# Kernel optimization log

Hardware: AMD Instinct MI355X
Metric: run time of the kernel (lower is better)

## Reference

```python
import jax, jax.numpy as jnp
import numpy as np

N_NODES = 50000
N_EDGES = 600000
D_IN = 128
D_OUT = 128
LN_EPS = 1e-5


def setup_inputs() -> dict:
    key = jax.random.key(0)
    ks = jax.random.split(key, 12)
    x = jax.random.normal(ks[0], (N_NODES, D_IN), dtype=jnp.float32)
    adj_in_rows = jax.random.randint(ks[1], (N_EDGES,), 0, N_NODES, dtype=jnp.int32)
    adj_in_cols = jax.random.randint(ks[2], (N_EDGES,), 0, N_NODES, dtype=jnp.int32)
    adj_in_vals = jax.random.uniform(ks[3], (N_EDGES,), dtype=jnp.float32)
    adj_out_rows = jax.random.randint(ks[4], (N_EDGES,), 0, N_NODES, dtype=jnp.int32)
    adj_out_cols = jax.random.randint(ks[5], (N_EDGES,), 0, N_NODES, dtype=jnp.int32)
    adj_out_vals = jax.random.uniform(ks[6], (N_EDGES,), dtype=jnp.float32)
    s = 1.0 / np.sqrt(D_IN)
    W_self = jax.random.uniform(ks[7], (D_OUT, D_IN), dtype=jnp.float32, minval=-s, maxval=s)
    b_self = jax.random.uniform(ks[8], (D_OUT,), dtype=jnp.float32, minval=-s, maxval=s)
    W_in = jax.random.uniform(ks[9], (D_OUT, D_IN), dtype=jnp.float32, minval=-s, maxval=s)
    W_out = jax.random.uniform(ks[10], (D_OUT, D_IN), dtype=jnp.float32, minval=-s, maxval=s)
    ln_gamma = jnp.ones((D_OUT,), dtype=jnp.float32)
    ln_beta = jnp.zeros((D_OUT,), dtype=jnp.float32)
    return {
        "x": x,
        "adj_in_rows": adj_in_rows, "adj_in_cols": adj_in_cols, "adj_in_vals": adj_in_vals,
        "adj_out_rows": adj_out_rows, "adj_out_cols": adj_out_cols, "adj_out_vals": adj_out_vals,
        "W_self": W_self, "b_self": b_self, "W_in": W_in, "W_out": W_out,
        "ln_gamma": ln_gamma, "ln_beta": ln_beta,
    }


def _spmm(rows, cols, vals, x, n):
    # COO sparse.mm: out[r] += vals[e] * x[cols[e]]
    return jax.ops.segment_sum(vals[:, None] * x[cols], rows, num_segments=n)


def reference(x, adj_in_rows, adj_in_cols, adj_in_vals,
              adj_out_rows, adj_out_cols, adj_out_vals,
              W_self, b_self, W_in, W_out, ln_gamma, ln_beta):
    n = x.shape[0]
    agg_in = _spmm(adj_in_rows, adj_in_cols, adj_in_vals, x, n)
    agg_out = _spmm(adj_out_rows, adj_out_cols, adj_out_vals, x, n)
    h = x @ W_self.T + b_self + agg_in @ W_in.T + agg_out @ W_out.T
    mu = jnp.mean(h, axis=-1, keepdims=True)
    var = jnp.mean(jnp.square(h - mu), axis=-1, keepdims=True)
    h = (h - mu) * jax.lax.rsqrt(var + LN_EPS) * ln_gamma + ln_beta
    # dropout is identity in eval mode (training=False)
    return jax.nn.relu(h)
```

## Files before the change

kernel.cpp:

```cpp
#include <hip/hip_runtime.h>

#define N_NODES 50000
#define N_EDGES 600000
#define D 128
#define BM 32
#define NT (2 * N_NODES)
#define NE2 (2 * N_EDGES)
#define NPAD 50048
#define KA 384
#define GBM 64
#define NB 1563
#define BROWS 64
#define CAPE 1024
#define CHUNK_A 8192

typedef __attribute__((ext_vector_type(8))) short bf16x8;
typedef __attribute__((ext_vector_type(4))) float f32x4;

__device__ inline unsigned short bfr(float x) {
    unsigned b = __float_as_uint(x);
    b += 0x7FFFu + ((b >> 16) & 1u);
    return (unsigned short)(b >> 16);
}
__device__ inline float bf_lo(unsigned u) { return __uint_as_float(u << 16); }
__device__ inline float bf_hi(unsigned u) { return __uint_as_float(u & 0xFFFF0000u); }


__global__ __launch_bounds__(256) void cvt_x(const float* __restrict__ x, short* __restrict__ A)
{
    int gid = blockIdx.x * 256 + threadIdx.x;
    if (gid >= N_NODES * 32) return;
    int row = gid >> 5, c4 = gid & 31;
    float4 v = *reinterpret_cast<const float4*>(x + (size_t)row * D + c4 * 4);
    ushort4 o = { bfr(v.x), bfr(v.y), bfr(v.z), bfr(v.w) };
    *reinterpret_cast<ushort4*>(A + (size_t)row * KA + c4 * 4) = o;
}

__global__ __launch_bounds__(384) void cvt_w(
    const float* __restrict__ Ws, const float* __restrict__ Wi,
    const float* __restrict__ Wo, short* __restrict__ Wc)
{
    int j = blockIdx.x, k = threadIdx.x;
    float v = (k < 128) ? Ws[j * 128 + k]
            : (k < 256) ? Wi[j * 128 + k - 128]
                        : Wo[j * 128 + k - 256];
    Wc[j * KA + k] = (short)bfr(v);
}


__global__ __launch_bounds__(1024) void bucket_hist(
    const int* __restrict__ ir, const int* __restrict__ orow, int* __restrict__ bcnt)
{
    __shared__ int h[NB];
    for (int i = threadIdx.x; i < NB; i += 1024) h[i] = 0;
    __syncthreads();
    int stride = gridDim.x * 1024;
    for (int e = blockIdx.x * 1024 + threadIdx.x; e < NE2; e += stride) {
        int r = (e < N_EDGES) ? ir[e] : N_NODES + orow[e - N_EDGES];
        atomicAdd(&h[r >> 6], 1);
    }
    __syncthreads();
    for (int i = threadIdx.x; i < NB; i += 1024)
        if (h[i]) atomicAdd(&bcnt[i], h[i]);
}

__global__ __launch_bounds__(1024) void scan_buckets(
    const int* __restrict__ bcnt, int* __restrict__ bbase, int* __restrict__ bcur)
{
    __shared__ int s[1024];
    const int t = threadIdx.x;
    const int i0 = 2 * t, i1 = 2 * t + 1;
    int v0 = (i0 < NB) ? bcnt[i0] : 0;
    int v1 = (i1 < NB) ? bcnt[i1] : 0;
    int v = v0 + v1;
    s[t] = v;
    __syncthreads();
    for (int o = 1; o < 1024; o <<= 1) {
        int u = (t >= o) ? s[t - o] : 0;
        __syncthreads();
        s[t] += u;
        __syncthreads();
    }
    int ex = s[t] - v;
    if (i0 < NB) { bbase[i0] = ex;      bcur[i0] = ex; }
    if (i1 < NB) { bbase[i1] = ex + v0; bcur[i1] = ex + v0; }
}

__global__ __launch_bounds__(1024) void scatter_buckets(
    const int* __restrict__ ir, const int* __restrict__ icol, const float* __restrict__ ival,
    const int* __restrict__ orow, const int* __restrict__ ocol, const float* __restrict__ oval,
    int* __restrict__ bcur, int2* __restrict__ pairp)
{
    __shared__ int hist[NB];
    __shared__ int cur[NB];
    const int t = threadIdx.x;
    for (int i = t; i < NB; i += 1024) hist[i] = 0;
    __syncthreads();

    const int e0 = blockIdx.x * CHUNK_A;
    int rr[8], cc[8]; float vv[8];
#pragma unroll
    for (int i = 0; i < 8; ++i) {
        int e = e0 + t + i * 1024;
        if (e < N_EDGES)      { rr[i] = ir[e];                       cc[i] = icol[e];           vv[i] = ival[e]; }
        else if (e < NE2)     { rr[i] = N_NODES + orow[e - N_EDGES]; cc[i] = ocol[e - N_EDGES]; vv[i] = oval[e - N_EDGES]; }
        else                  { rr[i] = -1; cc[i] = 0; vv[i] = 0.f; }
        if (rr[i] >= 0) atomicAdd(&hist[rr[i] >> 6], 1);
    }
    __syncthreads();
    for (int i = t; i < NB; i += 1024) {
        int c = hist[i];
        cur[i] = c ? atomicAdd(&bcur[i], c) : 0;
    }
    __syncthreads();
#pragma unroll
    for (int i = 0; i < 8; ++i) {
        if (rr[i] < 0) continue;
        int pos = atomicAdd(&cur[rr[i] >> 6], 1);
        pairp[pos] = make_int2((cc[i] & 0xFFFF) | ((rr[i] & 63) << 16), __float_as_int(vv[i]));
    }
}

__global__ __launch_bounds__(256) void bucket_spmm(
    const int* __restrict__ bbase, const int* __restrict__ bcnt,
    const int2* __restrict__ pairp, short* __restrict__ A)
{
    __shared__ int2 ed[CAPE];
    __shared__ int  rs[BROWS];
    __shared__ int  rstart[BROWS + 1];
    __shared__ int  rcur[BROWS];

    const int t = threadIdx.x;
    const int b = blockIdx.x;
    const int base = bbase[b];
    const int n = bcnt[b];
    const int w = t >> 6, lane = t & 63;
    const int row0 = w * 16;
    const char* Ab = (const char*)A + lane * 4;

    float ax[16], ay[16];
#pragma unroll
    for (int i = 0; i < 16; ++i) { ax[i] = 0.f; ay[i] = 0.f; }

    for (int s0 = 0; s0 < n; s0 += CAPE) {
        const int m = min(n - s0, CAPE);
        if (t < BROWS) rs[t] = 0;
        __syncthreads();
        int2 myp[4];
#pragma unroll
        for (int k = 0; k < 4; ++k) {
            int i = t + k * 256;
            if (i < m) {
                myp[k] = pairp[base + s0 + i];
                atomicAdd(&rs[(myp[k].x >> 16) & 63], 1);
            }
        }
        __syncthreads();
        if (t < 64) {
            int v = rs[t];
            int acc = v;
#pragma unroll
            for (int o = 1; o < 64; o <<= 1) {
                int u = __shfl_up(acc, o);
                if (t >= o) acc += u;
            }
            rstart[t] = acc - v;
            rcur[t]   = acc - v;
            if (t == 63) rstart[64] = acc;
        }
        __syncthreads();
#pragma unroll
        for (int k = 0; k < 4; ++k) {
            int i = t + k * 256;
            if (i < m) {
                int pos = atomicAdd(&rcur[(myp[k].x >> 16) & 63], 1);
                ed[pos] = myp[k];
            }
        }
        __syncthreads();
#pragma unroll
        for (int ri = 0; ri < 16; ++ri) {
            const int r = row0 + ri;
            int i = rstart[r];
            const int e2 = rstart[r + 1];
            float lax = ax[ri], lay = ay[ri];
            for (; i + 3 < e2; i += 4) {
                int2 p0 = ed[i], p1 = ed[i + 1], p2 = ed[i + 2], p3 = ed[i + 3];
                unsigned u0 = *(const unsigned*)(Ab + (unsigned)((p0.x & 0xFFFF) * (KA * 2)));
                unsigned u1 = *(const unsigned*)(Ab + (unsigned)((p1.x & 0xFFFF) * (KA * 2)));
                unsigned u2 = *(const unsigned*)(Ab + (unsigned)((p2.x & 0xFFFF) * (KA * 2)));
                unsigned u3 = *(const unsigned*)(Ab + (unsigned)((p3.x & 0xFFFF) * (KA * 2)));
                float v0 = __int_as_float(p0.y), v1 = __int_as_float(p1.y);
                float v2 = __int_as_float(p2.y), v3 = __int_as_float(p3.y);
                lax += v0 * bf_lo(u0) + v1 * bf_lo(u1) + v2 * bf_lo(u2) + v3 * bf_lo(u3);
                lay += v0 * bf_hi(u0) + v1 * bf_hi(u1) + v2 * bf_hi(u2) + v3 * bf_hi(u3);
            }
            for (; i < e2; ++i) {
                int2 p = ed[i];
                float v = __int_as_float(p.y);
                unsigned u = *(const unsigned*)(Ab + (unsigned)((p.x & 0xFFFF) * (KA * 2)));
                lax += v * bf_lo(u);
                lay += v * bf_hi(u);
            }
            ax[ri] = lax; ay[ri] = lay;
        }
        __syncthreads();
    }

    char* Aw = (char*)A;
#pragma unroll
    for (int ri = 0; ri < 16; ++ri) {
        int wv = b * BROWS + row0 + ri;
        if (wv >= NT) continue;
        unsigned o = ((unsigned)bfr(ay[ri]) << 16) | (unsigned)bfr(ax[ri]);
        size_t dst = (wv < N_NODES)
                   ? ((size_t)wv * (KA * 2) + 256 + lane * 4)
                   : ((size_t)(wv - N_NODES) * (KA * 2) + 512 + lane * 4);
        *(unsigned*)(Aw + dst) = o;
    }
}

__global__ __launch_bounds__(512) void gemm_mfma(
    const short* __restrict__ A, const short* __restrict__ Wc,
    const float* __restrict__ b, const float* __restrict__ gamma,
    const float* __restrict__ beta, float* __restrict__ out)
{
    __shared__ short Alds[GBM * KA];
    __shared__ float red[8][64][2];
    __shared__ float2 mustd[64];

    const int t = threadIdx.x;
    const int l = t & 63, w = t >> 6;
    const int q = l >> 4, c = l & 15;
    const int base = blockIdx.x * GBM;

    bf16x8 bfrag[12];
    const short* wrow = Wc + (size_t)(w * 16 + c) * KA + q * 8;
#pragma unroll
    for (int s = 0; s < 12; ++s)
        bfrag[s] = *reinterpret_cast<const bf16x8*>(wrow + s * 32);

#pragma unroll
    for (int i = 0; i < 6; ++i) {
        int slot = t + i * 512;
        int row = slot / 48, c16 = slot % 48;
        bf16x8 v = *reinterpret_cast<const bf16x8*>(A + (size_t)(base + row) * KA + c16 * 8);
        *reinterpret_cast<bf16x8*>(&Alds[row * KA + (c16 ^ (row & 7)) * 8]) = v;
    }
    __syncthreads();

    f32x4 acc[4];
#pragma unroll
    for (int rg = 0; rg < 4; ++rg) acc[rg] = (f32x4){0.f, 0.f, 0.f, 0.f};

#pragma unroll
    for (int s = 0; s < 12; ++s) {
#pragma unroll
        for (int rg = 0; rg < 4; ++rg) {
            int row = rg * 16 + c;
            int c16 = (s * 4 + q) ^ (row & 7);
            bf16x8 af = *reinterpret_cast<const bf16x8*>(&Alds[row * KA + c16 * 8]);
            acc[rg] = __builtin_amdgcn_mfma_f32_16x16x32_bf16(af, bfrag[s], acc[rg], 0, 0, 0);
        }
    }

    const float bj = b[w * 16 + c];
    const float gj = gamma[w * 16 + c];
    const float ej = beta[w * 16 + c];

#pragma unroll
    for (int rg = 0; rg < 4; ++rg) {
#pragma unroll
        for (int r = 0; r < 4; ++r) {
            float hv = acc[rg][r] + bj;
            acc[rg][r] = hv;
            float s1 = hv, s2 = hv * hv;
#pragma unroll
            for (int m = 1; m < 16; m <<= 1) {
                s1 += __shfl_xor(s1, m);
                s2 += __shfl_xor(s2, m);
            }
            if (c == 0) {
                int row = rg * 16 + q * 4 + r;
                red[w][row][0] = s1;
                red[w][row][1] = s2;
            }
        }
    }
    __syncthreads();

    if (t < 64) {
        float s1 = 0.f, s2 = 0.f;
#pragma unroll
        for (int ww = 0; ww < 8; ++ww) { s1 += red[ww][t][0]; s2 += red[ww][t][1]; }
        float mu = s1 * (1.f / 128.f);
        float var = s2 * (1.f / 128.f) - mu * mu;
        mustd[t] = make_float2(mu, rsqrtf(var + 1e-5f));
    }
    __syncthreads();

#pragma unroll
    for (int rg = 0; rg < 4; ++rg) {
        int row0 = rg * 16 + q * 4;
        int node0 = base + row0;
#pragma unroll
        for (int r = 0; r < 4; ++r) {
            float2 ms = mustd[row0 + r];
            float y = (acc[rg][r] - ms.x) * ms.y * gj + ej;
            y = fmaxf(y, 0.f);
            if (node0 + r < N_NODES)
                out[(size_t)(node0 + r) * D + w * 16 + c] = y;
        }
    }
}

__global__ __launch_bounds__(256) void spmm_scatter(
    const int* __restrict__ rows, const int* __restrict__ cols,
    const float* __restrict__ vals, const float* __restrict__ x,
    float* __restrict__ agg, int nE)
{
    int g = blockIdx.x * 256 + threadIdx.x;
    int e = g >> 5;
    if (e >= nE) return;
    int q = g & 31;
    int r = rows[e], c = cols[e];
    float v = vals[e];
    float4 xv = *reinterpret_cast<const float4*>(x + (size_t)c * D + (size_t)q * 4);
    float* ap = agg + (size_t)r * D + (size_t)q * 4;
    atomicAdd(ap + 0, v * xv.x);
    atomicAdd(ap + 1, v * xv.y);
    atomicAdd(ap + 2, v * xv.z);
    atomicAdd(ap + 3, v * xv.w);
}

__global__ __launch_bounds__(256) void gemm_ln_relu(
    const float* __restrict__ x, const float* __restrict__ agg_in,
    const float* __restrict__ agg_out,
    const float* __restrict__ Ws, const float* __restrict__ Wi,
    const float* __restrict__ Wo, const float* __restrict__ b,
    const float* __restrict__ gamma, const float* __restrict__ beta,
    float* __restrict__ out, int n)
{
    __shared__ float4 Wl[D * (D / 4)];
    __shared__ float4 Xl[BM * (D / 4)];

    const int t = threadIdx.x;
    const int l = t & 63;
    const int w = t >> 6;
    const int base = blockIdx.x * BM;
    const int j0 = l, j1 = l + 64;

    float acc0[8], acc1[8];
    const float bj0 = b[j0], bj1 = b[j1];
#pragma unroll
    for (int i = 0; i < 8; ++i) { acc0[i] = bj0; acc1[i] = bj1; }

    const float* srcs[3] = { x, agg_in, agg_out };
    const float* wms[3]  = { Ws, Wi, Wo };

#pragma unroll
    for (int s = 0; s < 3; ++s) {
        const float4* src4 = reinterpret_cast<const float4*>(srcs[s]);
        const float4* w4   = reinterpret_cast<const float4*>(wms[s]);
        __syncthreads();
#pragma unroll
        for (int it = 0; it < 16; ++it) {
            int gi = t + 256 * it;
            int j = gi >> 5, k4 = gi & 31;
            Wl[j * 32 + (k4 ^ (j & 7))] = w4[gi];
        }
#pragma unroll
        for (int it = 0; it < 4; ++it) {
            int gi = t + 256 * it;
            int m = gi >> 5, k4 = gi & 31;
            int node = base + m;
            float4 v = (node < n) ? src4[(size_t)node * 32 + k4]
                                  : make_float4(0.f, 0.f, 0.f, 0.f);
            Xl[m * 32 + k4] = v;
        }
        __syncthreads();

        const int sw = j0 & 7;
#pragma unroll 8
        for (int k4 = 0; k4 < 32; ++k4) {
            float4 w0 = Wl[j0 * 32 + (k4 ^ sw)];
            float4 w1 = Wl[j1 * 32 + (k4 ^ sw)];
#pragma unroll
            for (int i = 0; i < 8; ++i) {
                float4 xv = Xl[(w + 4 * i) * 32 + k4];
                acc0[i] += xv.x * w0.x + xv.y * w0.y + xv.z * w0.z + xv.w * w0.w;
                acc1[i] += xv.x * w1.x + xv.y * w1.y + xv.z * w1.z + xv.w * w1.w;
            }
        }
    }

    const float g0 = gamma[j0], g1 = gamma[j1];
    const float be0 = beta[j0], be1 = beta[j1];
#pragma unroll
    for (int i = 0; i < 8; ++i) {
        int node = base + w + 4 * i;
        float s  = acc0[i] + acc1[i];
        float ss = acc0[i] * acc0[i] + acc1[i] * acc1[i];
#pragma unroll
        for (int off = 32; off; off >>= 1) {
            s  += __shfl_xor(s, off);
            ss += __shfl_xor(ss, off);
        }
        float mu   = s * (1.0f / D);
        float var  = ss * (1.0f / D) - mu * mu;
        float rstd = rsqrtf(var + 1e-5f);
        if (node < n) {
            float y0 = (acc0[i] - mu) * rstd * g0 + be0;
            float y1 = (acc1[i] - mu) * rstd * g1 + be1;
            out[(size_t)node * D + j0] = fmaxf(y0, 0.f);
            out[(size_t)node * D + j1] = fmaxf(y1, 0.f);
        }
    }
}

extern "C" void kernel_launch(void* const* d_in, const int* in_sizes, int n_in,
                              void* d_out, int out_size, void* d_ws, size_t ws_size,
                              hipStream_t stream) {
    const float* x     = (const float*)d_in[0];
    const int*   ir    = (const int*)  d_in[1];
    const int*   icoln = (const int*)  d_in[2];
    const float* ival  = (const float*)d_in[3];
    const int*   orow  = (const int*)  d_in[4];
    const int*   ocol  = (const int*)  d_in[5];
    const float* oval  = (const float*)d_in[6];
    const float* Ws    = (const float*)d_in[7];
    const float* b     = (const float*)d_in[8];
    const float* Wi    = (const float*)d_in[9];
    const float* Wo    = (const float*)d_in[10];
    const float* gamma = (const float*)d_in[11];
    const float* beta  = (const float*)d_in[12];
    float* out = (float*)d_out;

    short* A     = (short*)d_ws;
    short* Wc    = A + (size_t)NPAD * KA;
    int*   bcnt  = (int*)(Wc + (size_t)128 * KA);
    int*   bbase = bcnt + NB;
    int*   bcur  = bbase + NB;
    int2*  pairp = (int2*)(bcur + NB + ((3 * NB) & 1));
    size_t need  = (size_t)NPAD * KA * 2 + (size_t)128 * KA * 2
                 + (size_t)(3 * NB + 2) * 4 + (size_t)NE2 * 8;

    if (ws_size >= need) {
        hipMemsetAsync(bcnt, 0, NB * sizeof(int), stream);
        hipMemsetAsync(A + (size_t)N_NODES * KA, 0,
                       (size_t)(NPAD - N_NODES) * KA * 2, stream);

        cvt_x<<<(N_NODES * 32 + 255) / 256, 256, 0, stream>>>(x, A);
        cvt_w<<<128, 384, 0, stream>>>(Ws, Wi, Wo, Wc);

        bucket_hist<<<128, 1024, 0, stream>>>(ir, orow, bcnt);
        scan_buckets<<<1, 1024, 0, stream>>>(bcnt, bbase, bcur);
        scatter_buckets<<<(NE2 + CHUNK_A - 1) / CHUNK_A, 1024, 0, stream>>>(
            ir, icoln, ival, orow, ocol, oval, bcur, pairp);
        bucket_spmm<<<NB, 256, 0, stream>>>(bbase, bcnt, pairp, A);

        gemm_mfma<<<NPAD / GBM, 512, 0, stream>>>(A, Wc, b, gamma, beta, out);
    } else {
        float* agg_in  = (float*)d_ws;
        float* agg_out = agg_in + (size_t)N_NODES * D;
        hipMemsetAsync(d_ws, 0, 2 * (size_t)N_NODES * D * sizeof(float), stream);
        const int eblocks = (N_EDGES * 32 + 255) / 256;
        spmm_scatter<<<eblocks, 256, 0, stream>>>(ir, icoln, ival, x, agg_in, N_EDGES);
        spmm_scatter<<<eblocks, 256, 0, stream>>>(orow, ocol, oval, x, agg_out, N_EDGES);
        const int gblocks = (N_NODES + BM - 1) / BM;
        gemm_ln_relu<<<gblocks, 256, 0, stream>>>(x, agg_in, agg_out, Ws, Wi, Wo,
                                                  b, gamma, beta, out, N_NODES);
    }
}
```

Before: 145.5 us.

## Stage bucket scatter in LDS and widen SpMM gathers to 8-byte loads

scatter_buckets now sorts each chunk's edges by bucket in shared memory, using a block-local scan and a per-bucket global base, then writes the pairs out in bucket order, so global stores land in contiguous runs instead of random positions. bucket_spmm moves to 512 threads: each wave covers 8 rows, and its two half-waves split a row's edges, each lane loading 4 bf16 features (8 bytes) per edge, with the halves combined by a cross-half shuffle. The aim is better coalescing on both scatter writes and gathers, at the cost of more shared memory (about 100KB in scatter) and some wasted, clamped loads on rows with few edges.

```diff
diff --git a/kernel.cpp b/kernel.cpp
--- a/kernel.cpp
+++ b/kernel.cpp
@@ -91,13 +91,19 @@
     const int* __restrict__ orow, const int* __restrict__ ocol, const float* __restrict__ oval,
     int* __restrict__ bcur, int2* __restrict__ pairp)
 {
-    __shared__ int hist[NB];
-    __shared__ int cur[NB];
+    __shared__ int2 pay[CHUNK_A];
+    __shared__ int  dstp[CHUNK_A];
+    __shared__ int  hist[NB];
+    __shared__ int  lofs[NB];
+    __shared__ int  gb2[NB];
+    __shared__ int  sbuf[1024];
+
     const int t = threadIdx.x;
     for (int i = t; i < NB; i += 1024) hist[i] = 0;
     __syncthreads();
 
     const int e0 = blockIdx.x * CHUNK_A;
+    const int m = min(NE2 - e0, CHUNK_A);
     int rr[8], cc[8]; float vv[8];
 #pragma unroll
     for (int i = 0; i < 8; ++i) {
@@ -108,20 +114,48 @@
         if (rr[i] >= 0) atomicAdd(&hist[rr[i] >> 6], 1);
     }
     __syncthreads();
+
+    const int i0 = 2 * t, i1 = 2 * t + 1;
+    int h0 = (i0 < NB) ? hist[i0] : 0;
+    int h1 = (i1 < NB) ? hist[i1] : 0;
+    int hv = h0 + h1;
+    sbuf[t] = hv;
+    __syncthreads();
+    for (int o = 1; o < 1024; o <<= 1) {
+        int u = (t >= o) ? sbuf[t - o] : 0;
+        __syncthreads();
+        sbuf[t] += u;
+        __syncthreads();
+    }
+    int ex = sbuf[t] - hv;
+    if (i0 < NB) lofs[i0] = ex;
+    if (i1 < NB) lofs[i1] = ex + h0;
+    __syncthreads();
+
     for (int i = t; i < NB; i += 1024) {
         int c = hist[i];
-        cur[i] = c ? atomicAdd(&bcur[i], c) : 0;
-    }
-    __syncthreads();
+        int g = c ? atomicAdd(&bcur[i], c) : 0;
+        gb2[i] = g - lofs[i];
+    }
+    __syncthreads();
+    for (int i = t; i < NB; i += 1024) hist[i] = lofs[i];
+    __syncthreads();
+
 #pragma unroll
     for (int i = 0; i < 8; ++i) {
         if (rr[i] < 0) continue;
-        int pos = atomicAdd(&cur[rr[i] >> 6], 1);
-        pairp[pos] = make_int2((cc[i] & 0xFFFF) | ((rr[i] & 63) << 16), __float_as_int(vv[i]));
-    }
-}
-
-__global__ __launch_bounds__(256) void bucket_spmm(
+        int bk = rr[i] >> 6;
+        int s = atomicAdd(&hist[bk], 1);
+        pay[s]  = make_int2((cc[i] & 0xFFFF) | ((rr[i] & 63) << 16), __float_as_int(vv[i]));
+        dstp[s] = gb2[bk] + s;
+    }
+    __syncthreads();
+
+    for (int i = t; i < m; i += 1024)
+        pairp[dstp[i]] = pay[i];
+}
+
+__global__ __launch_bounds__(512) void bucket_spmm(
     const int* __restrict__ bbase, const int* __restrict__ bcnt,
     const int2* __restrict__ pairp, short* __restrict__ A)
 {
@@ -135,21 +169,22 @@
     const int base = bbase[b];
     const int n = bcnt[b];
     const int w = t >> 6, lane = t & 63;
-    const int row0 = w * 16;
-    const char* Ab = (const char*)A + lane * 4;
-
-    float ax[16], ay[16];
-#pragma unroll
-    for (int i = 0; i < 16; ++i) { ax[i] = 0.f; ay[i] = 0.f; }
+    const int h = lane >> 5, sl = lane & 31;
+    const int row0 = w * 8;
+    const char* Ab = (const char*)A + sl * 8;
+
+    float4 acc[8];
+#pragma unroll
+    for (int i = 0; i < 8; ++i) acc[i] = make_float4(0.f, 0.f, 0.f, 0.f);
 
     for (int s0 = 0; s0 < n; s0 += CAPE) {
         const int m = min(n - s0, CAPE);
         if (t < BROWS) rs[t] = 0;
         __syncthreads();
-        int2 myp[4];
-#pragma unroll
-        for (int k = 0; k < 4; ++k) {
-            int i = t + k * 256;
+        int2 myp[2];
+#pragma unroll
+        for (int k = 0; k < 2; ++k) {
+            int i = t + k * 512;
             if (i < m) {
                 myp[k] = pairp[base + s0 + i];
                 atomicAdd(&rs[(myp[k].x >> 16) & 63], 1);
@@ -158,20 +193,20 @@
         __syncthreads();
         if (t < 64) {
             int v = rs[t];
-            int acc = v;
+            int a = v;
 #pragma unroll
             for (int o = 1; o < 64; o <<= 1) {
-                int u = __shfl_up(acc, o);
-                if (t >= o) acc += u;
-            }
-            rstart[t] = acc - v;
-            rcur[t]   = acc - v;
-            if (t == 63) rstart[64] = acc;
-        }
-        __syncthreads();
-#pragma unroll
-        for (int k = 0; k < 4; ++k) {
-            int i = t + k * 256;
+                int u = __shfl_up(a, o);
+                if (t >= o) a += u;
+            }
+            rstart[t] = a - v;
+            rcur[t]   = a - v;
+            if (t == 63) rstart[64] = a;
+        }
+        __syncthreads();
+#pragma unroll
+        for (int k = 0; k < 2; ++k) {
+            int i = t + k * 512;
             if (i < m) {
                 int pos = atomicAdd(&rcur[(myp[k].x >> 16) & 63], 1);
                 ed[pos] = myp[k];
@@ -179,44 +214,46 @@
         }
         __syncthreads();
 #pragma unroll
-        for (int ri = 0; ri < 16; ++ri) {
+        for (int ri = 0; ri < 8; ++ri) {
             const int r = row0 + ri;
-            int i = rstart[r];
-            const int e2 = rstart[r + 1];
-            float lax = ax[ri], lay = ay[ri];
-            for (; i + 3 < e2; i += 4) {
-                int2 p0 = ed[i], p1 = ed[i + 1], p2 = ed[i + 2], p3 = ed[i + 3];
-                unsigned u0 = *(const unsigned*)(Ab + (unsigned)((p0.x & 0xFFFF) * (KA * 2)));
-                unsigned u1 = *(const unsigned*)(Ab + (unsigned)((p1.x & 0xFFFF) * (KA * 2)));
-                unsigned u2 = *(const unsigned*)(Ab + (unsigned)((p2.x & 0xFFFF) * (KA * 2)));
-                unsigned u3 = *(const unsigned*)(Ab + (unsigned)((p3.x & 0xFFFF) * (KA * 2)));
-                float v0 = __int_as_float(p0.y), v1 = __int_as_float(p1.y);
-                float v2 = __int_as_float(p2.y), v3 = __int_as_float(p3.y);
-                lax += v0 * bf_lo(u0) + v1 * bf_lo(u1) + v2 * bf_lo(u2) + v3 * bf_lo(u3);
-                lay += v0 * bf_hi(u0) + v1 * bf_hi(u1) + v2 * bf_hi(u2) + v3 * bf_hi(u3);
-            }
-            for (; i < e2; ++i) {
-                int2 p = ed[i];
-                float v = __int_as_float(p.y);
-                unsigned u = *(const unsigned*)(Ab + (unsigned)((p.x & 0xFFFF) * (KA * 2)));
-                lax += v * bf_lo(u);
-                lay += v * bf_hi(u);
-            }
-            ax[ri] = lax; ay[ri] = lay;
+            const int s = rstart[r], e2 = rstart[r + 1];
+            float4 a = acc[ri];
+            for (int i = s; i < e2; i += 8) {
+#pragma unroll
+                for (int k = 0; k < 4; ++k) {
+                    int idx = i + 2 * k + h;
+                    int2 p = ed[min(idx, e2 - 1)];
+                    float v = (idx < e2) ? __int_as_float(p.y) : 0.f;
+                    uint2 u = *(const uint2*)(Ab + (unsigned)((p.x & 0xFFFF) * (KA * 2)));
+                    a.x += v * bf_lo(u.x);
+                    a.y += v * bf_hi(u.x);
+                    a.z += v * bf_lo(u.y);
+                    a.w += v * bf_hi(u.y);
+                }
+            }
+            acc[ri] = a;
         }
         __syncthreads();
     }
 
     char* Aw = (char*)A;
 #pragma unroll
-    for (int ri = 0; ri < 16; ++ri) {
+    for (int ri = 0; ri < 8; ++ri) {
+        float4 a = acc[ri];
+        a.x += __shfl_xor(a.x, 32);
+        a.y += __shfl_xor(a.y, 32);
+        a.z += __shfl_xor(a.z, 32);
+        a.w += __shfl_xor(a.w, 32);
         int wv = b * BROWS + row0 + ri;
-        if (wv >= NT) continue;
-        unsigned o = ((unsigned)bfr(ay[ri]) << 16) | (unsigned)bfr(ax[ri]);
-        size_t dst = (wv < N_NODES)
-                   ? ((size_t)wv * (KA * 2) + 256 + lane * 4)
-                   : ((size_t)(wv - N_NODES) * (KA * 2) + 512 + lane * 4);
-        *(unsigned*)(Aw + dst) = o;
+        if (lane < 32 && wv < NT) {
+            uint2 o;
+            o.x = ((unsigned)bfr(a.y) << 16) | (unsigned)bfr(a.x);
+            o.y = ((unsigned)bfr(a.w) << 16) | (unsigned)bfr(a.z);
+            size_t dst = (wv < N_NODES)
+                       ? ((size_t)wv * (KA * 2) + 256 + sl * 8)
+                       : ((size_t)(wv - N_NODES) * (KA * 2) + 512 + sl * 8);
+            *(uint2*)(Aw + dst) = o;
+        }
     }
 }
 
@@ -457,7 +494,7 @@
         scan_buckets<<<1, 1024, 0, stream>>>(bcnt, bbase, bcur);
         scatter_buckets<<<(NE2 + CHUNK_A - 1) / CHUNK_A, 1024, 0, stream>>>(
             ir, icoln, ival, orow, ocol, oval, bcur, pairp);
-        bucket_spmm<<<NB, 256, 0, stream>>>(bbase, bcnt, pairp, A);
+        bucket_spmm<<<NB, 512, 0, stream>>>(bbase, bcnt, pairp, A);
 
         gemm_mfma<<<NPAD / GBM, 512, 0, stream>>>(A, Wc, b, gamma, beta, out);
     } else {
```

Measured after the change: 137.9 us. -5.3%, faster.

## Split bucket SpMM into row sort plus wave-per-row gather, coalesce scatter

Applied to the files above, without the earlier changes.

The fused bucket SpMM kernel, where each wave walked 16 rows serially, is replaced by two kernels. A row_sort kernel builds a per-row CSR (row_ptr plus sorted pairs), and a gather_rows kernel gives each row its own wave, with an 8-way unrolled gather loop. The edge scatter now does a local counting sort of each chunk in LDS, so global writes go out grouped by bucket instead of as random single stores. The x and weight conversions and the zeroing memsets are folded into one prep kernel to cut launch count. The cost is an extra kernel launch and an extra full pass over the edge pair array, plus more workspace.

```diff
diff --git a/kernel.cpp b/kernel.cpp
--- a/kernel.cpp
+++ b/kernel.cpp
@@ -9,10 +9,9 @@
 #define NPAD 50048
 #define KA 384
 #define GBM 64
-#define NB 1563
-#define BROWS 64
-#define CAPE 1024
-#define CHUNK_A 8192
+#define NBB 1563
+#define CAPB 2048
+#define CHUNK_A 4096
 
 typedef __attribute__((ext_vector_type(8))) short bf16x8;
 typedef __attribute__((ext_vector_type(4))) float f32x4;
@@ -25,42 +24,59 @@
 __device__ inline float bf_lo(unsigned u) { return __uint_as_float(u << 16); }
 __device__ inline float bf_hi(unsigned u) { return __uint_as_float(u & 0xFFFF0000u); }
 
-
-__global__ __launch_bounds__(256) void cvt_x(const float* __restrict__ x, short* __restrict__ A)
-{
-    int gid = blockIdx.x * 256 + threadIdx.x;
-    if (gid >= N_NODES * 32) return;
-    int row = gid >> 5, c4 = gid & 31;
-    float4 v = *reinterpret_cast<const float4*>(x + (size_t)row * D + c4 * 4);
-    ushort4 o = { bfr(v.x), bfr(v.y), bfr(v.z), bfr(v.w) };
-    *reinterpret_cast<ushort4*>(A + (size_t)row * KA + c4 * 4) = o;
-}
-
-__global__ __launch_bounds__(384) void cvt_w(
-    const float* __restrict__ Ws, const float* __restrict__ Wi,
-    const float* __restrict__ Wo, short* __restrict__ Wc)
-{
-    int j = blockIdx.x, k = threadIdx.x;
-    float v = (k < 128) ? Ws[j * 128 + k]
-            : (k < 256) ? Wi[j * 128 + k - 128]
-                        : Wo[j * 128 + k - 256];
-    Wc[j * KA + k] = (short)bfr(v);
+#define G1 (NPAD * 32 / 256)
+#define G2 192
+#define NZI (NBB + 48 * 128)
+#define G3 ((NZI + 255) / 256)
+
+__global__ __launch_bounds__(256) void prep(
+    const float* __restrict__ x, const float* __restrict__ Ws,
+    const float* __restrict__ Wi, const float* __restrict__ Wo,
+    short* __restrict__ A, short* __restrict__ Wc, int* __restrict__ bcnt)
+{
+    const int bid = blockIdx.x, t = threadIdx.x;
+    if (bid < G1) {
+        int gid = bid * 256 + t;
+        int row = gid >> 5, c4 = gid & 31;
+        ushort4 o = {0, 0, 0, 0};
+        if (row < N_NODES) {
+            float4 v = *reinterpret_cast<const float4*>(x + (size_t)row * D + c4 * 4);
+            o.x = bfr(v.x); o.y = bfr(v.y); o.z = bfr(v.z); o.w = bfr(v.w);
+        }
+        *reinterpret_cast<ushort4*>(A + (size_t)row * KA + c4 * 4) = o;
+    } else if (bid < G1 + G2) {
+        int gid = (bid - G1) * 256 + t;
+        int j = gid / 384, k = gid - j * 384;
+        float v = (k < 128) ? Ws[j * 128 + k]
+                : (k < 256) ? Wi[j * 128 + k - 128]
+                            : Wo[j * 128 + k - 256];
+        Wc[j * KA + k] = (short)bfr(v);
+    } else {
+        int z = (bid - G1 - G2) * 256 + t;
+        if (z < NBB) bcnt[z] = 0;
+        else if (z < NZI) {
+            int z2 = z - NBB;
+            int row = N_NODES + (z2 >> 7);
+            int o = z2 & 127;
+            ((int*)A)[(size_t)row * (KA / 2) + 64 + o] = 0;
+        }
+    }
 }
 
 
 __global__ __launch_bounds__(1024) void bucket_hist(
     const int* __restrict__ ir, const int* __restrict__ orow, int* __restrict__ bcnt)
 {
-    __shared__ int h[NB];
-    for (int i = threadIdx.x; i < NB; i += 1024) h[i] = 0;
+    __shared__ int h[NBB];
+    for (int i = threadIdx.x; i < NBB; i += 1024) h[i] = 0;
     __syncthreads();
     int stride = gridDim.x * 1024;
     for (int e = blockIdx.x * 1024 + threadIdx.x; e < NE2; e += stride) {
-        int r = (e < N_EDGES) ? ir[e] : N_NODES + orow[e - N_EDGES];
-        atomicAdd(&h[r >> 6], 1);
-    }
-    __syncthreads();
-    for (int i = threadIdx.x; i < NB; i += 1024)
+        int rid = (e < N_EDGES) ? ir[e] : N_NODES + orow[e - N_EDGES];
+        atomicAdd(&h[rid >> 6], 1);
+    }
+    __syncthreads();
+    for (int i = threadIdx.x; i < NBB; i += 1024)
         if (h[i]) atomicAdd(&bcnt[i], h[i]);
 }
 
@@ -70,8 +86,8 @@
     __shared__ int s[1024];
     const int t = threadIdx.x;
     const int i0 = 2 * t, i1 = 2 * t + 1;
-    int v0 = (i0 < NB) ? bcnt[i0] : 0;
-    int v1 = (i1 < NB) ? bcnt[i1] : 0;
+    int v0 = (i0 < NBB) ? bcnt[i0] : 0;
+    int v1 = (i1 < NBB) ? bcnt[i1] : 0;
     int v = v0 + v1;
     s[t] = v;
     __syncthreads();
@@ -82,142 +98,172 @@
         __syncthreads();
     }
     int ex = s[t] - v;
-    if (i0 < NB) { bbase[i0] = ex;      bcur[i0] = ex; }
-    if (i1 < NB) { bbase[i1] = ex + v0; bcur[i1] = ex + v0; }
-}
-
-__global__ __launch_bounds__(1024) void scatter_buckets(
+    if (i0 < NBB) { bbase[i0] = ex;      bcur[i0] = ex; }
+    if (i1 < NBB) { bbase[i1] = ex + v0; bcur[i1] = ex + v0; }
+}
+
+__global__ __launch_bounds__(1024) void scatter_chunks(
     const int* __restrict__ ir, const int* __restrict__ icol, const float* __restrict__ ival,
     const int* __restrict__ orow, const int* __restrict__ ocol, const float* __restrict__ oval,
     int* __restrict__ bcur, int2* __restrict__ pairp)
 {
-    __shared__ int hist[NB];
-    __shared__ int cur[NB];
+    __shared__ int2 pay[CHUNK_A];
+    __shared__ int  dstp[CHUNK_A];
+    __shared__ int  hist[NBB];
+    __shared__ int  gb2[NBB];
+    __shared__ int  sbuf[1024];
+
     const int t = threadIdx.x;
-    for (int i = t; i < NB; i += 1024) hist[i] = 0;
+    for (int i = t; i < NBB; i += 1024) hist[i] = 0;
     __syncthreads();
 
     const int e0 = blockIdx.x * CHUNK_A;
-    int rr[8], cc[8]; float vv[8];
-#pragma unroll
-    for (int i = 0; i < 8; ++i) {
+    const int m = min(NE2 - e0, CHUNK_A);
+    int bk4[4], px4[4], vv4[4];
+#pragma unroll
+    for (int i = 0; i < 4; ++i) {
         int e = e0 + t + i * 1024;
-        if (e < N_EDGES)      { rr[i] = ir[e];                       cc[i] = icol[e];           vv[i] = ival[e]; }
-        else if (e < NE2)     { rr[i] = N_NODES + orow[e - N_EDGES]; cc[i] = ocol[e - N_EDGES]; vv[i] = oval[e - N_EDGES]; }
-        else                  { rr[i] = -1; cc[i] = 0; vv[i] = 0.f; }
-        if (rr[i] >= 0) atomicAdd(&hist[rr[i] >> 6], 1);
-    }
-    __syncthreads();
-    for (int i = t; i < NB; i += 1024) {
-        int c = hist[i];
-        cur[i] = c ? atomicAdd(&bcur[i], c) : 0;
-    }
-    __syncthreads();
-#pragma unroll
-    for (int i = 0; i < 8; ++i) {
-        if (rr[i] < 0) continue;
-        int pos = atomicAdd(&cur[rr[i] >> 6], 1);
-        pairp[pos] = make_int2((cc[i] & 0xFFFF) | ((rr[i] & 63) << 16), __float_as_int(vv[i]));
-    }
-}
-
-__global__ __launch_bounds__(256) void bucket_spmm(
+        int rid, col; float val;
+        if (e < N_EDGES)      { rid = ir[e];                       col = icol[e];            val = ival[e]; }
+        else if (e < NE2)     { rid = N_NODES + orow[e - N_EDGES]; col = ocol[e - N_EDGES];  val = oval[e - N_EDGES]; }
+        else                  { rid = -1; col = 0; val = 0.f; }
+        if (rid >= 0) {
+            bk4[i] = rid >> 6;
+            px4[i] = (col & 0xFFFF) | ((rid & 63) << 16);
+            vv4[i] = __float_as_int(val);
+            atomicAdd(&hist[bk4[i]], 1);
+        } else bk4[i] = -1;
+    }
+    __syncthreads();
+
+    const int i0 = 2 * t, i1 = 2 * t + 1;
+    int v0 = (i0 < NBB) ? hist[i0] : 0;
+    int v1 = (i1 < NBB) ? hist[i1] : 0;
+    int v = v0 + v1;
+    sbuf[t] = v;
+    __syncthreads();
+    for (int o = 1; o < 1024; o <<= 1) {
+        int u = (t >= o) ? sbuf[t - o] : 0;
+        __syncthreads();
+        sbuf[t] += u;
+        __syncthreads();
+    }
+    int ex = sbuf[t] - v;
+    if (i0 < NBB) {
+        int g = v0 ? atomicAdd(&bcur[i0], v0) : 0;
+        gb2[i0] = g - ex;
+        hist[i0] = ex;
+    }
+    if (i1 < NBB) {
+        int g = v1 ? atomicAdd(&bcur[i1], v1) : 0;
+        gb2[i1] = g - (ex + v0);
+        hist[i1] = ex + v0;
+    }
+    __syncthreads();
+
+#pragma unroll
+    for (int i = 0; i < 4; ++i) {
+        if (bk4[i] < 0) continue;
+        int s = atomicAdd(&hist[bk4[i]], 1);
+        pay[s]  = make_int2(px4[i], vv4[i]);
+        dstp[s] = gb2[bk4[i]] + s;
+    }
+    __syncthreads();
+
+    for (int i = t; i < m; i += 1024)
+        pairp[dstp[i]] = pay[i];
+}
+
+__global__ __launch_bounds__(256) void row_sort(
     const int* __restrict__ bbase, const int* __restrict__ bcnt,
-    const int2* __restrict__ pairp, short* __restrict__ A)
-{
-    __shared__ int2 ed[CAPE];
-    __shared__ int  rs[BROWS];
-    __shared__ int  rstart[BROWS + 1];
-    __shared__ int  rcur[BROWS];
-
-    const int t = threadIdx.x;
-    const int b = blockIdx.x;
+    const int2* __restrict__ pairp, int2* __restrict__ pairp2,
+    int* __restrict__ row_ptr)
+{
+    __shared__ int2 pay[CAPB];
+    __shared__ int  rs[64];
+    __shared__ int  rcur[64];
+
+    const int b = blockIdx.x, t = threadIdx.x;
     const int base = bbase[b];
     const int n = bcnt[b];
-    const int w = t >> 6, lane = t & 63;
-    const int row0 = w * 16;
+
+    if (t < 64) rs[t] = 0;
+    __syncthreads();
+
+    const bool fast = (n <= CAPB);
+    if (fast) {
+        for (int i = t; i < n; i += 256) {
+            int2 p = pairp[base + i];
+            pay[i] = p;
+            atomicAdd(&rs[(p.x >> 16) & 63], 1);
+        }
+    } else {
+        for (int i = t; i < n; i += 256)
+            atomicAdd(&rs[(pairp[base + i].x >> 16) & 63], 1);
+    }
+    __syncthreads();
+
+    if (t < 64) {
+        int v = rs[t];
+        int a = v;
+#pragma unroll
+        for (int o = 1; o < 64; o <<= 1) {
+            int u = __shfl_up(a, o);
+            if (t >= o) a += u;
+        }
+        int ex = a - v;
+        rcur[t] = ex;
+        row_ptr[b * 64 + t] = base + ex;
+    }
+    __syncthreads();
+
+    if (fast) {
+        for (int i = t; i < n; i += 256) {
+            int2 p = pay[i];
+            int pos = atomicAdd(&rcur[(p.x >> 16) & 63], 1);
+            pairp2[base + pos] = p;
+        }
+    } else {
+        for (int i = t; i < n; i += 256) {
+            int2 p = pairp[base + i];
+            int pos = atomicAdd(&rcur[(p.x >> 16) & 63], 1);
+            pairp2[base + pos] = p;
+        }
+    }
+}
+
+__global__ __launch_bounds__(256) void gather_rows(
+    const int* __restrict__ row_ptr, const int2* __restrict__ pairp2,
+    short* __restrict__ A)
+{
+    const int wv = blockIdx.x * 4 + (threadIdx.x >> 6);
+    if (wv >= NT) return;
+    const int lane = threadIdx.x & 63;
+    int s = row_ptr[wv];
+    int e = row_ptr[wv + 1];
+    s = __builtin_amdgcn_readfirstlane(s);
+    e = __builtin_amdgcn_readfirstlane(e);
+
     const char* Ab = (const char*)A + lane * 4;
-
-    float ax[16], ay[16];
-#pragma unroll
-    for (int i = 0; i < 16; ++i) { ax[i] = 0.f; ay[i] = 0.f; }
-
-    for (int s0 = 0; s0 < n; s0 += CAPE) {
-        const int m = min(n - s0, CAPE);
-        if (t < BROWS) rs[t] = 0;
-        __syncthreads();
-        int2 myp[4];
-#pragma unroll
-        for (int k = 0; k < 4; ++k) {
-            int i = t + k * 256;
-            if (i < m) {
-                myp[k] = pairp[base + s0 + i];
-                atomicAdd(&rs[(myp[k].x >> 16) & 63], 1);
-            }
-        }
-        __syncthreads();
-        if (t < 64) {
-            int v = rs[t];
-            int acc = v;
-#pragma unroll
-            for (int o = 1; o < 64; o <<= 1) {
-                int u = __shfl_up(acc, o);
-                if (t >= o) acc += u;
-            }
-            rstart[t] = acc - v;
-            rcur[t]   = acc - v;
-            if (t == 63) rstart[64] = acc;
-        }
-        __syncthreads();
-#pragma unroll
-        for (int k = 0; k < 4; ++k) {
-            int i = t + k * 256;
-            if (i < m) {
-                int pos = atomicAdd(&rcur[(myp[k].x >> 16) & 63], 1);
-                ed[pos] = myp[k];
-            }
-        }
-        __syncthreads();
-#pragma unroll
-        for (int ri = 0; ri < 16; ++ri) {
-            const int r = row0 + ri;
-            int i = rstart[r];
-            const int e2 = rstart[r + 1];
-            float lax = ax[ri], lay = ay[ri];
-            for (; i + 3 < e2; i += 4) {
-                int2 p0 = ed[i], p1 = ed[i + 1], p2 = ed[i + 2], p3 = ed[i + 3];
-                unsigned u0 = *(const unsigned*)(Ab + (unsigned)((p0.x & 0xFFFF) * (KA * 2)));
-                unsigned u1 = *(const unsigned*)(Ab + (unsigned)((p1.x & 0xFFFF) * (KA * 2)));
-                unsigned u2 = *(const unsigned*)(Ab + (unsigned)((p2.x & 0xFFFF) * (KA * 2)));
-                unsigned u3 = *(const unsigned*)(Ab + (unsigned)((p3.x & 0xFFFF) * (KA * 2)));
-                float v0 = __int_as_float(p0.y), v1 = __int_as_float(p1.y);
-                float v2 = __int_as_float(p2.y), v3 = __int_as_float(p3.y);
-                lax += v0 * bf_lo(u0) + v1 * bf_lo(u1) + v2 * bf_lo(u2) + v3 * bf_lo(u3);
-                lay += v0 * bf_hi(u0) + v1 * bf_hi(u1) + v2 * bf_hi(u2) + v3 * bf_hi(u3);
-            }
-            for (; i < e2; ++i) {
-                int2 p = ed[i];
-                float v = __int_as_float(p.y);
-                unsigned u = *(const unsigned*)(Ab + (unsigned)((p.x & 0xFFFF) * (KA * 2)));
-                lax += v * bf_lo(u);
-                lay += v * bf_hi(u);
-            }
-            ax[ri] = lax; ay[ri] = lay;
-        }
-        __syncthreads();
-    }
-
-    char* Aw = (char*)A;
-#pragma unroll
-    for (int ri = 0; ri < 16; ++ri) {
-        int wv = b * BROWS + row0 + ri;
-        if (wv >= NT) continue;
-        unsigned o = ((unsigned)bfr(ay[ri]) << 16) | (unsigned)bfr(ax[ri]);
-        size_t dst = (wv < N_NODES)
-                   ? ((size_t)wv * (KA * 2) + 256 + lane * 4)
-                   : ((size_t)(wv - N_NODES) * (KA * 2) + 512 + lane * 4);
-        *(unsigned*)(Aw + dst) = o;
-    }
+    float ax = 0.f, ay = 0.f;
+
+    for (int i = s; i < e; i += 8) {
+#pragma unroll
+        for (int k = 0; k < 8; ++k) {
+            int idx = i + k;
+            int2 p = pairp2[min(idx, e - 1)];
+            float v = (idx < e) ? __int_as_float(p.y) : 0.f;
+            unsigned u = *(const unsigned*)(Ab + (unsigned)((p.x & 0xFFFF) * (KA * 2)));
+            ax += v * bf_lo(u);
+            ay += v * bf_hi(u);
+        }
+    }
+
+    unsigned o = ((unsigned)bfr(ay) << 16) | (unsigned)bfr(ax);
+    size_t dst = (wv < N_NODES)
+               ? ((size_t)wv * (KA * 2) + 256 + lane * 4)
+               : ((size_t)(wv - N_NODES) * (KA * 2) + 512 + lane * 4);
+    *(unsigned*)((char*)A + dst) = o;
 }
 
 __global__ __launch_bounds__(512) void gemm_mfma(
@@ -436,29 +482,26 @@
     const float* beta  = (const float*)d_in[12];
     float* out = (float*)d_out;
 
-    short* A     = (short*)d_ws;
-    short* Wc    = A + (size_t)NPAD * KA;
-    int*   bcnt  = (int*)(Wc + (size_t)128 * KA);
-    int*   bbase = bcnt + NB;
-    int*   bcur  = bbase + NB;
-    int2*  pairp = (int2*)(bcur + NB + ((3 * NB) & 1));
-    size_t need  = (size_t)NPAD * KA * 2 + (size_t)128 * KA * 2
-                 + (size_t)(3 * NB + 2) * 4 + (size_t)NE2 * 8;
+    short* A       = (short*)d_ws;
+    short* Wc      = A + (size_t)NPAD * KA;
+    int*   bcnt    = (int*)(Wc + (size_t)128 * KA);
+    int*   bbase   = bcnt + NBB;
+    int*   bcur    = bbase + NBB;
+    int*   row_ptr = bcur + NBB;
+    uintptr_t pp   = (uintptr_t)(row_ptr + NBB * 64 + 1);
+    pp = (pp + 7) & ~(uintptr_t)7;
+    int2*  pairp   = (int2*)pp;
+    int2*  pairp2  = pairp + NE2;
+    size_t need    = (size_t)((char*)(pairp2 + NE2) - (char*)d_ws);
 
     if (ws_size >= need) {
-        hipMemsetAsync(bcnt, 0, NB * sizeof(int), stream);
-        hipMemsetAsync(A + (size_t)N_NODES * KA, 0,
-                       (size_t)(NPAD - N_NODES) * KA * 2, stream);
-
-        cvt_x<<<(N_NODES * 32 + 255) / 256, 256, 0, stream>>>(x, A);
-        cvt_w<<<128, 384, 0, stream>>>(Ws, Wi, Wo, Wc);
-
+        prep<<<G1 + G2 + G3, 256, 0, stream>>>(x, Ws, Wi, Wo, A, Wc, bcnt);
         bucket_hist<<<128, 1024, 0, stream>>>(ir, orow, bcnt);
         scan_buckets<<<1, 1024, 0, stream>>>(bcnt, bbase, bcur);
-        scatter_buckets<<<(NE2 + CHUNK_A - 1) / CHUNK_A, 1024, 0, stream>>>(
+        scatter_chunks<<<(NE2 + CHUNK_A - 1) / CHUNK_A, 1024, 0, stream>>>(
             ir, icoln, ival, orow, ocol, oval, bcur, pairp);
-        bucket_spmm<<<NB, 256, 0, stream>>>(bbase, bcnt, pairp, A);
-
+        row_sort<<<NBB, 256, 0, stream>>>(bbase, bcnt, pairp, pairp2, row_ptr);
+        gather_rows<<<(NT + 3) / 4, 256, 0, stream>>>(row_ptr, pairp2, A);
         gemm_mfma<<<NPAD / GBM, 512, 0, stream>>>(A, Wc, b, gamma, beta, out);
     } else {
         float* agg_in  = (float*)d_ws;
```

Result: faster. 128.4 us (-11.7%).
